# Performance work log

Hardware: AMD Instinct MI355X
Metric: run time of the kernel (lower is better)

Reference implementation:

```python
import jax, jax.numpy as jnp
import numpy as np

DIM = 1024
ATT_DIM = 1024
BATCH = 16384


def setup_inputs() -> dict:
    key = jax.random.key(0)
    ks = jax.random.split(key, 10)
    inp = {
        "x": jax.random.normal(ks[0], (BATCH, DIM), dtype=jnp.float32),
        "last_x": jax.random.normal(ks[1], (BATCH, DIM), dtype=jnp.float32),
        "last_num": jax.random.normal(ks[2], (BATCH, ATT_DIM), dtype=jnp.float32),
        "last_den": jax.random.uniform(ks[3], (BATCH, ATT_DIM), dtype=jnp.float32) + 1.0,
        # learned parameters
        "mix_k": jnp.full((1, DIM), 0.5, dtype=jnp.float32),
        "mix_v": jnp.full((1, DIM), 0.5, dtype=jnp.float32),
        "mix_r": jnp.full((1, DIM), 0.5, dtype=jnp.float32),
        "decay": jnp.full((1, ATT_DIM), 0.5, dtype=jnp.float32),
        "bonus": jnp.full((1, ATT_DIM), 0.5, dtype=jnp.float32),
        "Wk": jax.random.normal(ks[4], (DIM, ATT_DIM), dtype=jnp.float32) * (DIM ** -0.5),
        "Wv": jax.random.normal(ks[5], (DIM, ATT_DIM), dtype=jnp.float32) * (DIM ** -0.5),
        "Wr": jax.random.normal(ks[6], (DIM, ATT_DIM), dtype=jnp.float32) * (DIM ** -0.5),
        "Wout": jax.random.normal(ks[7], (ATT_DIM, DIM), dtype=jnp.float32) * (ATT_DIM ** -0.5),
    }
    return inp


def reference(x, last_x, last_num, last_den, mix_k, mix_v, mix_r, decay, bonus,
              Wk, Wv, Wr, Wout):
    # interpolated token-shift mixing, then thin projections
    k = (x * mix_k + last_x * (1.0 - mix_k)) @ Wk          # [B, A]
    v = (x * mix_v + last_x * (1.0 - mix_v)) @ Wv          # [B, A]
    r = jax.nn.sigmoid((x * mix_r + last_x * (1.0 - mix_r)) @ Wr)  # [B, A]

    ebk = jnp.exp(bonus + k)                                # [B, A]
    wkv = (last_num + ebk * v) / (last_den + ebk)
    rwkv = r * wkv

    w = jnp.exp(-jnp.exp(decay))                            # [1, A]
    ek = jnp.exp(k)
    num = w * last_num + ek * v
    den = w * last_den + ek

    hidden = rwkv @ Wout                                    # [B, D]
    return (hidden, x, num, den)
```

## Files before the change

### kernel.cpp

```cpp
#include <hip/hip_runtime.h>
#include <stdint.h>


typedef __bf16 bf16;
typedef __bf16 bf16x8 __attribute__((ext_vector_type(8)));
typedef float  f32x4  __attribute__((ext_vector_type(4)));

#define BATCH 16384
#define DIM   1024
#define ADIM  1024
#define FP32_MAGIC 0x3F000000u

__device__ __forceinline__ void loadbf8(const bf16* p, float* d) {
  bf16x8 a = *(const bf16x8*)p;
#pragma unroll
  for (int e = 0; e < 8; ++e) d[e] = (float)a[e];
}
__device__ __forceinline__ void storebf8(bf16* p, const float* d) {
  bf16x8 a;
#pragma unroll
  for (int e = 0; e < 8; ++e) a[e] = (bf16)d[e];
  *(bf16x8*)p = a;
}

template <typename T> struct V8;
template <> struct V8<float> {
  __device__ static void load(const float* p, float* d) {
    f32x4 a = *(const f32x4*)p; f32x4 b = *(const f32x4*)(p + 4);
#pragma unroll
    for (int e = 0; e < 4; ++e) { d[e] = a[e]; d[e + 4] = b[e]; }
  }
  __device__ static void store(float* p, const float* d) {
    f32x4 a, b;
#pragma unroll
    for (int e = 0; e < 4; ++e) { a[e] = d[e]; b[e] = d[e + 4]; }
    *(f32x4*)p = a; *(f32x4*)(p + 4) = b;
  }
};
template <> struct V8<bf16> {
  __device__ static void load(const bf16* p, float* d) { loadbf8(p, d); }
  __device__ static void store(bf16* p, const float* d) { storebf8(p, d); }
};

__device__ __forceinline__ void async_copy16(const bf16* g, bf16* l) {
  __builtin_amdgcn_global_load_lds((const __attribute__((address_space(1))) void*)g,
                                   (__attribute__((address_space(3))) void*)l,
                                   16, 0, 0);
}

#define SCHED0 __builtin_amdgcn_sched_barrier(0)

template <typename TOut>
__device__ __forceinline__ void gemm_body8(const bf16* __restrict__ A, int lda,
                                           const bf16* __restrict__ BT,
                                           TOut* __restrict__ C,
                                           char* sm, int mtile, int ntile)
{
  constexpr int NT = 16;
  const int tid  = threadIdx.x;
  const int wave = tid >> 6;
  const int lane = tid & 63;
  const int wm = wave >> 2;
  const int wn = wave & 3;
  const long m0 = (long)mtile * 256;
  const long n0 = (long)ntile * 256;

  const int csrc  = (lane & 7) ^ (lane >> 3);
  const int rbase = wave * 16 + (lane >> 3) + ((wave >= 4) ? 64 : 0);
  const int cbase = (wave >> 1) * 64 + (wave & 1) * 16 + (lane >> 3);
  const bf16* pA = A  + (size_t)(m0 + rbase) * lda  + csrc * 8;
  const bf16* pB = BT + (size_t)(n0 + cbase) * 1024 + csrc * 8;
  char* const dA = sm + wave * 2048;
  char* const dB = sm + 32768 + wave * 2048;

  const int fr = lane & 15;
  const int fs = lane >> 4;
  const int c0 = ((fs ^ (fr & 7)) << 4);
  const int c1 = (((fs ^ 4) ^ (fr & 7)) << 4);
  const int raA = (wm * 64 + fr) * 128;
  const int raB = 32768 + (wn * 32 + fr) * 128;

  f32x4 acc[8][4] = {};

#define STAGE_A(tau, u) { \
    char* d_ = dA + (((tau) & 1) << 16) + (u) * 16384; \
    const bf16* s_ = pA + (size_t)((u) * 64) * lda + (size_t)(tau) * 64; \
    async_copy16(s_,           (bf16*)d_); \
    async_copy16(s_ + 8 * lda, (bf16*)(d_ + 1024)); }
#define STAGE_B(tau, u) { \
    char* d_ = dB + (((tau) & 1) << 16) + (u) * 16384; \
    const bf16* s_ = pB + (size_t)((u) * 32) * 1024 + (size_t)(tau) * 64; \
    async_copy16(s_,            (bf16*)d_); \
    async_copy16(s_ + 8 * 1024, (bf16*)(d_ + 1024)); }

  STAGE_A(0, 0); STAGE_A(0, 1); STAGE_B(0, 0); STAGE_B(0, 1);
  STAGE_A(1, 0); STAGE_A(1, 1); STAGE_B(1, 0);
  asm volatile("s_waitcnt vmcnt(6)" ::: "memory");
  __builtin_amdgcn_s_barrier();
  SCHED0;

#pragma unroll 2
  for (int t = 0; t < NT; ++t) {
    char* const sb = sm + ((t & 1) << 16);
    bf16x8 a0[4][2], a1[4][2], bq[2][2];

#pragma unroll
    for (int mf = 0; mf < 4; ++mf) {
      a0[mf][0] = *(const bf16x8*)(sb + raA + mf * 2048 + c0);
      a0[mf][1] = *(const bf16x8*)(sb + raA + mf * 2048 + c1);
    }
#pragma unroll
    for (int nf = 0; nf < 2; ++nf) {
      bq[nf][0] = *(const bf16x8*)(sb + raB + nf * 2048 + c0);
      bq[nf][1] = *(const bf16x8*)(sb + raB + nf * 2048 + c1);
    }
    SCHED0;
    if (t + 1 < NT) STAGE_B(t + 1, 1);
#pragma unroll
    for (int mf = 0; mf < 4; ++mf) {
      a1[mf][0] = *(const bf16x8*)(sb + raA + 16384 + mf * 2048 + c0);
      a1[mf][1] = *(const bf16x8*)(sb + raA + 16384 + mf * 2048 + c1);
    }
    SCHED0;
    __builtin_amdgcn_s_setprio(1);
#pragma unroll
    for (int kk = 0; kk < 2; ++kk)
#pragma unroll
      for (int mf = 0; mf < 4; ++mf)
#pragma unroll
        for (int nf = 0; nf < 2; ++nf)
          acc[mf][nf] = __builtin_amdgcn_mfma_f32_16x16x32_bf16(
              a0[mf][kk], bq[nf][kk], acc[mf][nf], 0, 0, 0);
#pragma unroll
    for (int kk = 0; kk < 2; ++kk)
#pragma unroll
      for (int mf = 0; mf < 4; ++mf)
#pragma unroll
        for (int nf = 0; nf < 2; ++nf)
          acc[4 + mf][nf] = __builtin_amdgcn_mfma_f32_16x16x32_bf16(
              a1[mf][kk], bq[nf][kk], acc[4 + mf][nf], 0, 0, 0);
    __builtin_amdgcn_s_setprio(0);
    __builtin_amdgcn_s_barrier();
    SCHED0;
#pragma unroll
    for (int nf = 0; nf < 2; ++nf) {
      bq[nf][0] = *(const bf16x8*)(sb + raB + 16384 + nf * 2048 + c0);
      bq[nf][1] = *(const bf16x8*)(sb + raB + 16384 + nf * 2048 + c1);
    }
    SCHED0;
    if (t + 2 < NT) { STAGE_A(t + 2, 0); STAGE_A(t + 2, 1); STAGE_B(t + 2, 0); }
    SCHED0;
    __builtin_amdgcn_s_setprio(1);
#pragma unroll
    for (int kk = 0; kk < 2; ++kk)
#pragma unroll
      for (int mf = 0; mf < 4; ++mf)
#pragma unroll
        for (int nf = 0; nf < 2; ++nf)
          acc[mf][2 + nf] = __builtin_amdgcn_mfma_f32_16x16x32_bf16(
              a0[mf][kk], bq[nf][kk], acc[mf][2 + nf], 0, 0, 0);
#pragma unroll
    for (int kk = 0; kk < 2; ++kk)
#pragma unroll
      for (int mf = 0; mf < 4; ++mf)
#pragma unroll
        for (int nf = 0; nf < 2; ++nf)
          acc[4 + mf][2 + nf] = __builtin_amdgcn_mfma_f32_16x16x32_bf16(
              a1[mf][kk], bq[nf][kk], acc[4 + mf][2 + nf], 0, 0, 0);
    __builtin_amdgcn_s_setprio(0);
    if (t < NT - 2)       { asm volatile("s_waitcnt vmcnt(6)" ::: "memory"); }
    else if (t == NT - 2) { asm volatile("s_waitcnt vmcnt(0)" ::: "memory"); }
    __builtin_amdgcn_s_barrier();
    SCHED0;
  }
#undef STAGE_A
#undef STAGE_B

  const int cl = fr, rq = fs * 4;
#pragma unroll
  for (int mf = 0; mf < 8; ++mf)
#pragma unroll
    for (int nf = 0; nf < 4; ++nf) {
      const size_t rb = (size_t)(m0 + wm * 128 + mf * 16 + rq) * 1024
                      + (size_t)(n0 + wn * 64 + nf * 16 + cl);
#pragma unroll
      for (int r = 0; r < 4; ++r)
        C[rb + (size_t)r * 1024] = (TOut)acc[mf][nf][r];
    }
}

__device__ __forceinline__ void swz_tiles(int& mtile, int& ntile) {
  const int nbx = gridDim.x, nwg = gridDim.x * gridDim.y;
  int flat = blockIdx.x + blockIdx.y * nbx;
  if ((nwg & 7) == 0 && nwg >= 16) {
    const int cpx = nwg >> 3;
    flat = (flat & 7) * cpx + (flat >> 3);
  }
  ntile = flat % nbx; mtile = flat / nbx;
}

__global__ __launch_bounds__(512, 2) void gemm3_kernel(
    const void* outbase, const bf16* __restrict__ xs,
    const bf16* __restrict__ WkT, const bf16* __restrict__ WvT, const bf16* __restrict__ WrT,
    bf16* kk, bf16* vv, bf16* rp, const uint32_t* probe, long r0)
{
  __shared__ char sm[131072];
  int mtile, ntile; swz_tiles(mtile, ntile);
  const int z = blockIdx.z;
  const bf16* BT = (z == 0) ? WkT : (z == 1) ? WvT : WrT;
  bf16*       Cz = (z == 0) ? kk  : (z == 1) ? vv  : rp;
  const bf16* Az; int lda;
  if (xs) {
    Az  = xs + (size_t)z * BATCH * 1024 + (size_t)r0 * 1024;
    lda = 1024;
  } else {
    const bool f32 = (*probe == FP32_MAGIC);
    const size_t es = f32 ? 4 : 2;
    const size_t reg = (z == 0) ? 0 : (z == 1) ? 2 : 3;
    Az  = (const bf16*)((const char*)outbase + reg * (size_t)BATCH * 1024 * es
                        + (size_t)r0 * 1024 * es);
    lda = (int)(512 * es);
  }
  gemm_body8<bf16>(Az, lda, BT, Cz, sm, mtile, ntile);
}

__global__ __launch_bounds__(512, 2) void gemm1_kernel(
    const bf16* __restrict__ rwkv, const bf16* __restrict__ WoT,
    void* outbase, const uint32_t* probe, long r0)
{
  __shared__ char sm[131072];
  int mtile, ntile; swz_tiles(mtile, ntile);
  if (*probe == FP32_MAGIC)
    gemm_body8<float>(rwkv, 1024, WoT, (float*)outbase + (size_t)r0 * 1024, sm, mtile, ntile);
  else
    gemm_body8<bf16>(rwkv, 1024, WoT, (bf16*)outbase + (size_t)r0 * 1024, sm, mtile, ntile);
}

template <typename T>
__device__ __forceinline__ void transpose_body(const T* W, bf16* WT, float (*t)[33]) {
  const int tx = threadIdx.x & 31, ty = threadIdx.x >> 5;
  const int x0 = blockIdx.x * 32, y0 = blockIdx.y * 32;
#pragma unroll
  for (int i = 0; i < 32; i += 8)
    t[ty + i][tx] = (float)W[(size_t)(y0 + ty + i) * 1024 + x0 + tx];
  __syncthreads();
#pragma unroll
  for (int i = 0; i < 32; i += 8)
    WT[(size_t)(x0 + ty + i) * 1024 + y0 + tx] = (bf16)t[tx][ty + i];
}

__global__ __launch_bounds__(256) void transpose4_kernel(
    const void* Wk, const void* Wv, const void* Wr, const void* Wo,
    bf16* WT0, const uint32_t* probe)
{
  __shared__ float t[32][33];
  const int z = blockIdx.z;
  const void* W = (z == 0) ? Wk : (z == 1) ? Wv : (z == 2) ? Wr : Wo;
  bf16* WT = WT0 + (size_t)z * DIM * ADIM;
  if (*probe == FP32_MAGIC) transpose_body<float>((const float*)W, WT, t);
  else                      transpose_body<bf16>((const bf16*)W, WT, t);
}

template <typename T>
__device__ __forceinline__ void mix_body(const T* x, const T* lx,
                                         const T* mk, const T* mv, const T* mr,
                                         char* outbase, bf16* xs)
{
  const size_t i8  = ((size_t)blockIdx.x * 256 + threadIdx.x) * 8;
  const size_t row = i8 >> 10;
  const int    col = (int)(i8 & 1023);
  constexpr size_t es = sizeof(T);
  const size_t BDes = (size_t)BATCH * 1024 * es;
  bf16 *xk, *xv, *xr;
  if (xs) {
    const size_t BD = (size_t)BATCH * 1024;
    xk = xs + i8; xv = xs + BD + i8; xr = xs + 2 * BD + i8;
  } else {
    const size_t rowb = row * 1024 * es;
    xk = (bf16*)(outbase + 0 * BDes + rowb) + col;
    xv = (bf16*)(outbase + 2 * BDes + rowb) + col;
    xr = (bf16*)(outbase + 3 * BDes + rowb) + col;
  }
  T* xout = (T*)(outbase + 1 * BDes) + i8;

  float a[8], b[8], k[8], v[8], r[8], ok[8], ov[8], orr[8];
  V8<T>::load(x + i8, a);
  V8<T>::load(lx + i8, b);
  V8<T>::load(mk + col, k);
  V8<T>::load(mv + col, v);
  V8<T>::load(mr + col, r);
#pragma unroll
  for (int e = 0; e < 8; ++e) {
    ok[e]  = a[e] * k[e] + b[e] * (1.0f - k[e]);
    ov[e]  = a[e] * v[e] + b[e] * (1.0f - v[e]);
    orr[e] = a[e] * r[e] + b[e] * (1.0f - r[e]);
  }
  storebf8(xk, ok);
  storebf8(xv, ov);
  storebf8(xr, orr);
  V8<T>::store(xout, a);
}

__global__ __launch_bounds__(256) void mix_kernel(
    const void* x, const void* lx, const void* mk, const void* mv, const void* mr,
    void* outbase, bf16* xs, const uint32_t* probe)
{
  if (*probe == FP32_MAGIC)
    mix_body<float>((const float*)x, (const float*)lx, (const float*)mk,
                    (const float*)mv, (const float*)mr, (char*)outbase, xs);
  else
    mix_body<bf16>((const bf16*)x, (const bf16*)lx, (const bf16*)mk,
                   (const bf16*)mv, (const bf16*)mr, (char*)outbase, xs);
}

template <typename T>
__device__ __forceinline__ void ew2_body(bf16* kk, const bf16* vv, const bf16* rp,
                                         const T* ln, const T* ld,
                                         const T* decay, const T* bonus,
                                         T* numo, T* deno, long grow0)
{
  const size_t li  = ((size_t)blockIdx.x * 256 + threadIdx.x) * 8;
  const size_t gi  = (size_t)grow0 + li;
  const int    col = (int)(gi & (ADIM - 1));
  float k[8], v[8], rr[8], n[8], d[8], de[8], bo[8];
  loadbf8(kk + li, k);
  loadbf8(vv + li, v);
  loadbf8(rp + li, rr);
  V8<T>::load(ln + gi, n);
  V8<T>::load(ld + gi, d);
  V8<T>::load(decay + col, de);
  V8<T>::load(bonus + col, bo);
  float orw[8], onu[8], ode[8];
#pragma unroll
  for (int e = 0; e < 8; ++e) {
    const float r   = 1.0f / (1.0f + __expf(-rr[e]));
    const float ebk = __expf(bo[e] + k[e]);
    const float wkv = (n[e] + ebk * v[e]) / (d[e] + ebk);
    orw[e] = r * wkv;
    const float w  = __expf(-__expf(de[e]));
    const float ek = __expf(k[e]);
    onu[e] = w * n[e] + ek * v[e];
    ode[e] = w * d[e] + ek;
  }
  storebf8(kk + li, orw);
  V8<T>::store(numo + gi, onu);
  V8<T>::store(deno + gi, ode);
}

__global__ __launch_bounds__(256) void ew2_kernel(
    bf16* kk, const bf16* vv, const bf16* rp,
    const void* ln, const void* ld, const void* decay, const void* bonus,
    void* outbase, const uint32_t* probe, long r0)
{
  const long grow0 = r0 * 1024;
  const long BD = (long)BATCH * 1024;
  if (*probe == FP32_MAGIC) {
    float* o = (float*)outbase;
    ew2_body<float>(kk, vv, rp, (const float*)ln, (const float*)ld,
                    (const float*)decay, (const float*)bonus,
                    o + 2 * BD, o + 3 * BD, grow0);
  } else {
    bf16* o = (bf16*)outbase;
    ew2_body<bf16>(kk, vv, rp, (const bf16*)ln, (const bf16*)ld,
                   (const bf16*)decay, (const bf16*)bonus,
                   o + 2 * BD, o + 3 * BD, grow0);
  }
}

extern "C" void kernel_launch(void* const* d_in, const int* in_sizes, int n_in,
                              void* d_out, int out_size, void* d_ws, size_t ws_size,
                              hipStream_t stream)
{
  const void* x     = d_in[0];
  const void* lx    = d_in[1];
  const void* ln    = d_in[2];
  const void* ld    = d_in[3];
  const void* mk    = d_in[4];
  const void* mv    = d_in[5];
  const void* mr    = d_in[6];
  const void* decay = d_in[7];
  const void* bonus = d_in[8];
  const void* Wk    = d_in[9];
  const void* Wv    = d_in[10];
  const void* Wr    = d_in[11];
  const void* Wo    = d_in[12];
  const uint32_t* probe = (const uint32_t*)d_in[4];

  bf16* WkT = (bf16*)d_ws;
  bf16* WvT = WkT + (size_t)DIM * ADIM;
  bf16* WrT = WvT + (size_t)DIM * ADIM;
  bf16* WoT = WrT + (size_t)DIM * ADIM;

  const size_t wt_bytes = 4ull * DIM * ADIM * sizeof(bf16);
  const size_t xs_bytes = 3ull * BATCH * DIM * sizeof(bf16);
  const size_t kv_bytes = 3ull * BATCH * ADIM * sizeof(bf16);

  bf16* xs = nullptr;
  bf16* kk;
  int chunk;
  if (ws_size >= wt_bytes + xs_bytes + kv_bytes) {
    xs = WoT + (size_t)DIM * ADIM;
    kk = xs + 3ull * BATCH * DIM;
    chunk = BATCH;
  } else {
    kk = WoT + (size_t)DIM * ADIM;
    const size_t avail = (ws_size > wt_bytes) ? ws_size - wt_bytes : 0;
    chunk = BATCH;
    while (chunk > 256 && (size_t)chunk * ADIM * sizeof(bf16) * 3 > avail) chunk >>= 1;
  }
  bf16* vv = kk + (size_t)chunk * ADIM;
  bf16* rp = vv + (size_t)chunk * ADIM;

  transpose4_kernel<<<dim3(32, 32, 4), 256, 0, stream>>>(Wk, Wv, Wr, Wo, WkT, probe);

  mix_kernel<<<(size_t)BATCH * DIM / 2048, 256, 0, stream>>>(x, lx, mk, mv, mr,
                                                             d_out, xs, probe);

  for (long r0 = 0; r0 < BATCH; r0 += chunk) {
    const dim3 g3(ADIM / 256, chunk / 256, 3);
    gemm3_kernel<<<g3, 512, 0, stream>>>(d_out, xs, WkT, WvT, WrT, kk, vv, rp, probe, r0);

    ew2_kernel<<<(size_t)chunk * ADIM / 2048, 256, 0, stream>>>(
        kk, vv, rp, ln, ld, decay, bonus, d_out, probe, r0);

    const dim3 g1(DIM / 256, chunk / 256);
    gemm1_kernel<<<g1, 512, 0, stream>>>(kk , WoT, d_out, probe, r0);
  }
}
```

Before: 643.3 us.

## Fuse whole pipeline into one cooperative persistent kernel with fused elementwise epilogue

Replaces the transpose, mix, three-projection GEMM, elementwise and output GEMM launches with a single cooperative kernel using grid-wide syncs between phases. The r projection's elementwise step (sigmoid, wkv, num/den updates) is fused into the GEMM epilogue, so the r activations are never written out. Launch overhead and one intermediate buffer round-trip are removed. In exchange the grid is capped at one block per CU, which halves occupancy relative to the two-blocks-per-CU launch bounds. The epilogue also does strided scalar loads and stores of k, v, last_num and last_den, with serial z-loop GEMMs per tile and no inter-tile overlap.

```diff
diff --git a/kernel.cpp b/kernel.cpp
--- a/kernel.cpp
+++ b/kernel.cpp
@@ -1,5 +1,8 @@
 #include <hip/hip_runtime.h>
+#include <hip/hip_cooperative_groups.h>
 #include <stdint.h>
+
+namespace cg = cooperative_groups;
 
 
 typedef __bf16 bf16;
@@ -50,20 +53,14 @@
 
 #define SCHED0 __builtin_amdgcn_sched_barrier(0)
 
-template <typename TOut>
-__device__ __forceinline__ void gemm_body8(const bf16* __restrict__ A, int lda,
-                                           const bf16* __restrict__ BT,
-                                           TOut* __restrict__ C,
-                                           char* sm, int mtile, int ntile)
+__device__ __forceinline__ void gemm_tile(const bf16* __restrict__ A, int lda,
+                                          const bf16* __restrict__ BT,
+                                          char* sm, long m0, long n0,
+                                          int wave, int lane, f32x4 (&acc)[8][4])
 {
   constexpr int NT = 16;
-  const int tid  = threadIdx.x;
-  const int wave = tid >> 6;
-  const int lane = tid & 63;
   const int wm = wave >> 2;
   const int wn = wave & 3;
-  const long m0 = (long)mtile * 256;
-  const long n0 = (long)ntile * 256;
 
   const int csrc  = (lane & 7) ^ (lane >> 3);
   const int rbase = wave * 16 + (lane >> 3) + ((wave >= 4) ? 64 : 0);
@@ -80,7 +77,10 @@
   const int raA = (wm * 64 + fr) * 128;
   const int raB = 32768 + (wn * 32 + fr) * 128;
 
-  f32x4 acc[8][4] = {};
+#pragma unroll
+  for (int i = 0; i < 8; ++i)
+#pragma unroll
+    for (int j = 0; j < 4; ++j) acc[i][j] = 0;
 
 #define STAGE_A(tau, u) { \
     char* d_ = dA + (((tau) & 1) << 16) + (u) * 16384; \
@@ -124,21 +124,21 @@
     SCHED0;
     __builtin_amdgcn_s_setprio(1);
 #pragma unroll
-    for (int kk = 0; kk < 2; ++kk)
+    for (int kk2 = 0; kk2 < 2; ++kk2)
 #pragma unroll
       for (int mf = 0; mf < 4; ++mf)
 #pragma unroll
         for (int nf = 0; nf < 2; ++nf)
           acc[mf][nf] = __builtin_amdgcn_mfma_f32_16x16x32_bf16(
-              a0[mf][kk], bq[nf][kk], acc[mf][nf], 0, 0, 0);
-#pragma unroll
-    for (int kk = 0; kk < 2; ++kk)
+              a0[mf][kk2], bq[nf][kk2], acc[mf][nf], 0, 0, 0);
+#pragma unroll
+    for (int kk2 = 0; kk2 < 2; ++kk2)
 #pragma unroll
       for (int mf = 0; mf < 4; ++mf)
 #pragma unroll
         for (int nf = 0; nf < 2; ++nf)
           acc[4 + mf][nf] = __builtin_amdgcn_mfma_f32_16x16x32_bf16(
-              a1[mf][kk], bq[nf][kk], acc[4 + mf][nf], 0, 0, 0);
+              a1[mf][kk2], bq[nf][kk2], acc[4 + mf][nf], 0, 0, 0);
     __builtin_amdgcn_s_setprio(0);
     __builtin_amdgcn_s_barrier();
     SCHED0;
@@ -152,21 +152,21 @@
     SCHED0;
     __builtin_amdgcn_s_setprio(1);
 #pragma unroll
-    for (int kk = 0; kk < 2; ++kk)
+    for (int kk2 = 0; kk2 < 2; ++kk2)
 #pragma unroll
       for (int mf = 0; mf < 4; ++mf)
 #pragma unroll
         for (int nf = 0; nf < 2; ++nf)
           acc[mf][2 + nf] = __builtin_amdgcn_mfma_f32_16x16x32_bf16(
-              a0[mf][kk], bq[nf][kk], acc[mf][2 + nf], 0, 0, 0);
-#pragma unroll
-    for (int kk = 0; kk < 2; ++kk)
+              a0[mf][kk2], bq[nf][kk2], acc[mf][2 + nf], 0, 0, 0);
+#pragma unroll
+    for (int kk2 = 0; kk2 < 2; ++kk2)
 #pragma unroll
       for (int mf = 0; mf < 4; ++mf)
 #pragma unroll
         for (int nf = 0; nf < 2; ++nf)
           acc[4 + mf][2 + nf] = __builtin_amdgcn_mfma_f32_16x16x32_bf16(
-              a1[mf][kk], bq[nf][kk], acc[4 + mf][2 + nf], 0, 0, 0);
+              a1[mf][kk2], bq[nf][kk2], acc[4 + mf][2 + nf], 0, 0, 0);
     __builtin_amdgcn_s_setprio(0);
     if (t < NT - 2)       { asm volatile("s_waitcnt vmcnt(6)" ::: "memory"); }
     else if (t == NT - 2) { asm volatile("s_waitcnt vmcnt(0)" ::: "memory"); }
@@ -175,8 +175,15 @@
   }
 #undef STAGE_A
 #undef STAGE_B
-
-  const int cl = fr, rq = fs * 4;
+}
+
+template <typename TOut>
+__device__ __forceinline__ void store_tile(TOut* C, long m0, long n0,
+                                           int wave, int lane,
+                                           const f32x4 (&acc)[8][4])
+{
+  const int wm = wave >> 2, wn = wave & 3;
+  const int cl = lane & 15, rq = (lane >> 4) * 4;
 #pragma unroll
   for (int mf = 0; mf < 8; ++mf)
 #pragma unroll
@@ -187,6 +194,173 @@
       for (int r = 0; r < 4; ++r)
         C[rb + (size_t)r * 1024] = (TOut)acc[mf][nf][r];
     }
+}
+
+template <typename T>
+__device__ __forceinline__ void fused_ew_tile(bf16* kk, const bf16* vv,
+    const T* ln, const T* ld, const T* decay, const T* bonus,
+    T* numo, T* deno, long m0, long n0, int wave, int lane,
+    const f32x4 (&acc)[8][4])
+{
+  const int wm = wave >> 2, wn = wave & 3;
+  const int cl = lane & 15, rq = (lane >> 4) * 4;
+#pragma unroll
+  for (int nf = 0; nf < 4; ++nf) {
+    const long col = n0 + wn * 64 + nf * 16 + cl;
+    const float bo = (float)bonus[col];
+    const float w  = __expf(-__expf((float)decay[col]));
+#pragma unroll
+    for (int mf = 0; mf < 8; ++mf) {
+      const long rowb = m0 + wm * 128 + mf * 16 + rq;
+#pragma unroll
+      for (int r = 0; r < 4; ++r) {
+        const size_t idx = (size_t)(rowb + r) * 1024 + col;
+        const float k = (float)kk[idx];
+        const float v = (float)vv[idx];
+        const float n = (float)ln[idx];
+        const float d = (float)ld[idx];
+        const float rs  = 1.0f / (1.0f + __expf(-acc[mf][nf][r]));
+        const float ebk = __expf(bo + k);
+        kk[idx] = (bf16)(rs * (n + ebk * v) / (d + ebk));
+        const float ek = __expf(k);
+        numo[idx] = (T)(w * n + ek * v);
+        deno[idx] = (T)(w * d + ek);
+      }
+    }
+  }
+}
+
+template <typename T>
+__device__ void mono_body(const T* x, const T* lx, const T* ln, const T* ld,
+                          const T* mk, const T* mv, const T* mr,
+                          const T* decay, const T* bonus,
+                          const T* Wk, const T* Wv, const T* Wr, const T* Wo,
+                          char* outbase, bf16* WT0, bf16* xs, bf16* kk, bf16* vv,
+                          char* sm)
+{
+  const int tid = threadIdx.x;
+  const int bid = blockIdx.x;
+  const int nb  = gridDim.x;
+  const size_t BD = (size_t)BATCH * 1024;
+  constexpr size_t es = sizeof(T);
+
+  {
+    float (*tt)[33] = (float(*)[33])sm;
+    const int tx = tid & 31, ty = tid >> 5;
+    for (int j = bid; j < 4096; j += nb) {
+      const int z = j >> 10, tl = j & 1023;
+      const int x0 = (tl & 31) * 32, y0 = (tl >> 5) * 32;
+      const T* W = (z == 0) ? Wk : (z == 1) ? Wv : (z == 2) ? Wr : Wo;
+      bf16* WT = WT0 + (size_t)z * DIM * ADIM;
+#pragma unroll
+      for (int i = 0; i < 32; i += 16)
+        tt[ty + i][tx] = (float)W[(size_t)(y0 + ty + i) * 1024 + x0 + tx];
+      __syncthreads();
+#pragma unroll
+      for (int i = 0; i < 32; i += 16)
+        WT[(size_t)(x0 + ty + i) * 1024 + y0 + tx] = (bf16)tt[tx][ty + i];
+      __syncthreads();
+    }
+  }
+  {
+    T* xout = (T*)(outbase + 1 * BD * es);
+    const size_t NV = BD / 8;
+    for (size_t jv = (size_t)bid * 512 + tid; jv < NV; jv += (size_t)nb * 512) {
+      const size_t i8 = jv * 8;
+      const int col = (int)(i8 & 1023);
+      float a[8], b[8], k[8], v[8], r[8], ok[8], ov[8], orr[8];
+      V8<T>::load(x + i8, a);
+      V8<T>::load(lx + i8, b);
+      V8<T>::load(mk + col, k);
+      V8<T>::load(mv + col, v);
+      V8<T>::load(mr + col, r);
+#pragma unroll
+      for (int e = 0; e < 8; ++e) {
+        ok[e]  = a[e] * k[e] + b[e] * (1.0f - k[e]);
+        ov[e]  = a[e] * v[e] + b[e] * (1.0f - v[e]);
+        orr[e] = a[e] * r[e] + b[e] * (1.0f - r[e]);
+      }
+      storebf8(xs + i8, ok);
+      storebf8(xs + BD + i8, ov);
+      storebf8(xs + 2 * BD + i8, orr);
+      V8<T>::store(xout + i8, a);
+    }
+  }
+  cg::this_grid().sync();
+
+  {
+    const int wave = tid >> 6, lane = tid & 63;
+    T* numo = (T*)(outbase + 2 * BD * es);
+    T* deno = (T*)(outbase + 3 * BD * es);
+#pragma unroll 1
+    for (int tj = bid; tj < 256; tj += nb) {
+      const int tl = (tj & 7) * 32 + (tj >> 3);
+      const long m0 = (long)(tl >> 2) * 256;
+      const long n0 = (long)(tl & 3) * 256;
+      f32x4 acc[8][4];
+#pragma unroll 1
+      for (int z = 0; z < 3; ++z) {
+        const bf16* Az  = xs  + (size_t)z * BD;
+        const bf16* BTz = WT0 + (size_t)z * DIM * ADIM;
+        gemm_tile(Az, 1024, BTz, sm, m0, n0, wave, lane, acc);
+        if (z == 0)      store_tile<bf16>(kk, m0, n0, wave, lane, acc);
+        else if (z == 1) store_tile<bf16>(vv, m0, n0, wave, lane, acc);
+        else fused_ew_tile<T>(kk, vv, ln, ld, decay, bonus, numo, deno,
+                              m0, n0, wave, lane, acc);
+      }
+    }
+  }
+  cg::this_grid().sync();
+
+  {
+    const int wave = tid >> 6, lane = tid & 63;
+    T* H = (T*)outbase;
+#pragma unroll 1
+    for (int tj = bid; tj < 256; tj += nb) {
+      const int tl = (tj & 7) * 32 + (tj >> 3);
+      const long m0 = (long)(tl >> 2) * 256;
+      const long n0 = (long)(tl & 3) * 256;
+      f32x4 acc[8][4];
+      gemm_tile(kk, 1024, WT0 + 3ull * DIM * ADIM, sm, m0, n0, wave, lane, acc);
+      store_tile<T>(H, m0, n0, wave, lane, acc);
+    }
+  }
+}
+
+__global__ __launch_bounds__(512, 2) void mono_kernel(
+    const void* x, const void* lx, const void* ln, const void* ld,
+    const void* mk, const void* mv, const void* mr,
+    const void* decay, const void* bonus,
+    const void* Wk, const void* Wv, const void* Wr, const void* Wo,
+    void* outbase, bf16* WT0, bf16* xs, bf16* kk, bf16* vv,
+    const uint32_t* probe)
+{
+  __shared__ char sm[131072];
+  if (*probe == FP32_MAGIC)
+    mono_body<float>((const float*)x, (const float*)lx, (const float*)ln,
+                     (const float*)ld, (const float*)mk, (const float*)mv,
+                     (const float*)mr, (const float*)decay, (const float*)bonus,
+                     (const float*)Wk, (const float*)Wv, (const float*)Wr,
+                     (const float*)Wo, (char*)outbase, WT0, xs, kk, vv, sm);
+  else
+    mono_body<bf16>((const bf16*)x, (const bf16*)lx, (const bf16*)ln,
+                    (const bf16*)ld, (const bf16*)mk, (const bf16*)mv,
+                    (const bf16*)mr, (const bf16*)decay, (const bf16*)bonus,
+                    (const bf16*)Wk, (const bf16*)Wv, (const bf16*)Wr,
+                    (const bf16*)Wo, (char*)outbase, WT0, xs, kk, vv, sm);
+}
+
+template <typename TOut>
+__device__ __forceinline__ void gemm_body8(const bf16* __restrict__ A, int lda,
+                                           const bf16* __restrict__ BT,
+                                           TOut* __restrict__ C,
+                                           char* sm, int mtile, int ntile)
+{
+  const int wave = threadIdx.x >> 6, lane = threadIdx.x & 63;
+  const long m0 = (long)mtile * 256, n0 = (long)ntile * 256;
+  f32x4 acc[8][4];
+  gemm_tile(A, lda, BT, sm, m0, n0, wave, lane, acc);
+  store_tile<TOut>(C, m0, n0, wave, lane, acc);
 }
 
 __device__ __forceinline__ void swz_tiles(int& mtile, int& ntile) {
@@ -386,24 +560,50 @@
   const void* Wo    = d_in[12];
   const uint32_t* probe = (const uint32_t*)d_in[4];
 
-  bf16* WkT = (bf16*)d_ws;
-  bf16* WvT = WkT + (size_t)DIM * ADIM;
-  bf16* WrT = WvT + (size_t)DIM * ADIM;
-  bf16* WoT = WrT + (size_t)DIM * ADIM;
-
+  bf16* WT0 = (bf16*)d_ws;
   const size_t wt_bytes = 4ull * DIM * ADIM * sizeof(bf16);
   const size_t xs_bytes = 3ull * BATCH * DIM * sizeof(bf16);
-  const size_t kv_bytes = 3ull * BATCH * ADIM * sizeof(bf16);
+  const size_t BD = (size_t)BATCH * 1024;
+
+  static int s_coop = -2;
+  if (s_coop == -2) {
+    s_coop = -1;
+    hipDeviceProp_t prop{};
+    int bpc = 0;
+    if (hipGetDeviceProperties(&prop, 0) == hipSuccess && prop.cooperativeLaunch &&
+        hipOccupancyMaxActiveBlocksPerMultiprocessor(&bpc, mono_kernel, 512, 0)
+            == hipSuccess && bpc >= 1) {
+      int nb = prop.multiProcessorCount;
+      if (nb > 256) nb = 256;
+      if (nb >= 64) s_coop = nb;
+    }
+  }
+  const size_t mono_need = wt_bytes + xs_bytes + 2ull * BD * sizeof(bf16);
+  if (s_coop > 0 && ws_size >= mono_need) {
+    bf16* xs = WT0 + 4ull * DIM * ADIM;
+    bf16* kk = xs + 3ull * BD;
+    bf16* vv = kk + BD;
+    void* kargs[] = {
+      (void*)&x, (void*)&lx, (void*)&ln, (void*)&ld, (void*)&mk, (void*)&mv,
+      (void*)&mr, (void*)&decay, (void*)&bonus, (void*)&Wk, (void*)&Wv,
+      (void*)&Wr, (void*)&Wo, (void*)&d_out, (void*)&WT0, (void*)&xs,
+      (void*)&kk, (void*)&vv, (void*)&probe };
+    if (hipLaunchCooperativeKernel((const void*)mono_kernel, dim3(s_coop),
+                                   dim3(512), kargs, 0, stream) == hipSuccess)
+      return;
+    s_coop = -1;
+  }
 
   bf16* xs = nullptr;
   bf16* kk;
   int chunk;
+  const size_t kv_bytes = 3ull * BATCH * ADIM * sizeof(bf16);
   if (ws_size >= wt_bytes + xs_bytes + kv_bytes) {
-    xs = WoT + (size_t)DIM * ADIM;
-    kk = xs + 3ull * BATCH * DIM;
+    xs = WT0 + 4ull * DIM * ADIM;
+    kk = xs + 3ull * BD;
     chunk = BATCH;
   } else {
-    kk = WoT + (size_t)DIM * ADIM;
+    kk = WT0 + 4ull * DIM * ADIM;
     const size_t avail = (ws_size > wt_bytes) ? ws_size - wt_bytes : 0;
     chunk = BATCH;
     while (chunk > 256 && (size_t)chunk * ADIM * sizeof(bf16) * 3 > avail) chunk >>= 1;
@@ -411,19 +611,16 @@
   bf16* vv = kk + (size_t)chunk * ADIM;
   bf16* rp = vv + (size_t)chunk * ADIM;
 
-  transpose4_kernel<<<dim3(32, 32, 4), 256, 0, stream>>>(Wk, Wv, Wr, Wo, WkT, probe);
-
+  transpose4_kernel<<<dim3(32, 32, 4), 256, 0, stream>>>(Wk, Wv, Wr, Wo, WT0, probe);
   mix_kernel<<<(size_t)BATCH * DIM / 2048, 256, 0, stream>>>(x, lx, mk, mv, mr,
                                                              d_out, xs, probe);
-
   for (long r0 = 0; r0 < BATCH; r0 += chunk) {
     const dim3 g3(ADIM / 256, chunk / 256, 3);
-    gemm3_kernel<<<g3, 512, 0, stream>>>(d_out, xs, WkT, WvT, WrT, kk, vv, rp, probe, r0);
-
+    gemm3_kernel<<<g3, 512, 0, stream>>>(d_out, xs, WT0, WT0 + (size_t)DIM * ADIM,
+                                         WT0 + 2ull * DIM * ADIM, kk, vv, rp, probe, r0);
     ew2_kernel<<<(size_t)chunk * ADIM / 2048, 256, 0, stream>>>(
         kk, vv, rp, ln, ld, decay, bonus, d_out, probe, r0);
-
     const dim3 g1(DIM / 256, chunk / 256);
-    gemm1_kernel<<<g1, 512, 0, stream>>>(kk , WoT, d_out, probe, r0);
-  }
-}
+    gemm1_kernel<<<g1, 512, 0, stream>>>(kk, WT0 + 3ull * DIM * ADIM, d_out, probe, r0);
+  }
+}
```

New measurement: 644.8 us. No clear change (+0.2%).
